# Performance work log

Measured on AMD Instinct MI355X. Metric: run time of the kernel, lower is better.

The kernel has to match this reference:

```python
import jax, jax.numpy as jnp
import numpy as np

B, N, D = 4, 2048, 512
H, HD = 8, 64  # heads, output_dim per head


def setup_inputs() -> dict:
    key = jax.random.key(0)
    ks = jax.random.split(key, 6)
    x = jax.random.normal(ks[0], (B, N, D), dtype=jnp.float32)
    adj = (jax.random.uniform(ks[1], (N, N)) < 0.1).astype(jnp.float32)
    adj = jnp.maximum(adj, jnp.eye(N, dtype=jnp.float32))
    s = 0.02
    Wq = jax.random.normal(ks[2], (D, H * HD), dtype=jnp.float32) * s
    Wk = jax.random.normal(ks[3], (D, H * HD), dtype=jnp.float32) * s
    Wv = jax.random.normal(ks[4], (D, H * HD), dtype=jnp.float32) * s
    bq = jnp.zeros((H * HD,), dtype=jnp.float32)
    bk = jnp.zeros((H * HD,), dtype=jnp.float32)
    bv = jnp.zeros((H * HD,), dtype=jnp.float32)
    return {"x": x, "adj": adj, "Wq": Wq, "bq": bq, "Wk": Wk, "bk": bk, "Wv": Wv, "bv": bv}


def reference(x, adj, Wq, bq, Wk, bk, Wv, bv):
    b, n, _ = x.shape
    q = (x @ Wq + bq).reshape(b, n, H, HD)
    k = (x @ Wk + bk).reshape(b, n, H, HD)
    v = (x @ Wv + bv).reshape(b, n, H, HD)
    # scores: [b, h, i, j]
    scores = jnp.einsum('bihd,bjhd->bhij', q, k) / jnp.sqrt(jnp.float32(HD))
    mask = jnp.where(adj == 0, jnp.float32(-1e9), jnp.float32(0.0))  # [n, n]
    scores = scores + mask[None, None, :, :]
    weights = jax.nn.softmax(scores, axis=-1)
    # dropout is identity at inference (training=False)
    out = jnp.einsum('bhij,bjhd->bihd', weights, v)
    return out.reshape(b, n, H * HD)
```

## Files before the change

kernel.cpp:

```cpp
#include <hip/hip_runtime.h>
#include <hip/hip_bf16.h>
#include <stdint.h>

#define NTOK 2048
#define DIN  512
#define QSCALE 0.18033688011112042f

typedef __attribute__((ext_vector_type(8))) short bf16x8;
typedef __attribute__((ext_vector_type(4))) short bf16x4;
typedef __attribute__((ext_vector_type(4))) float f32x4;

#define MFMA16(a, b, c) __builtin_amdgcn_mfma_f32_16x16x32_bf16((a), (b), (c), 0, 0, 0)

union u4bf8 { uint4 u; bf16x8 h; };

static __device__ __forceinline__ short f2bf(float f) {
  union { float f; uint32_t u; } v; v.f = f;
  uint32_t r = (v.u + 0x7FFFu + ((v.u >> 16) & 1u)) >> 16;
  return (short)r;
}

__global__ __launch_bounds__(256) void k_xbf(const float* __restrict__ x, short* __restrict__ xb) {
  size_t i = (size_t)blockIdx.x * 256 + threadIdx.x;
  const float4 v = *(const float4*)(x + i * 4);
  bf16x4 h;
  h[0] = f2bf(v.x); h[1] = f2bf(v.y); h[2] = f2bf(v.z); h[3] = f2bf(v.w);
  *(bf16x4*)(xb + i * 4) = h;
}

__global__ __launch_bounds__(256) void k_wt(const float* __restrict__ Wq,
                                            const float* __restrict__ Wk,
                                            const float* __restrict__ Wv,
                                            short* __restrict__ Wt) {
  const float* W = (blockIdx.z == 0) ? Wq : ((blockIdx.z == 1) ? Wk : Wv);
  short* Wo = Wt + (size_t)blockIdx.z * DIN * DIN;
  __shared__ float tile[32][33];
  int bo = blockIdx.x * 32, bc = blockIdx.y * 32;
  int tx = threadIdx.x & 31, ty = threadIdx.x >> 5;
#pragma unroll
  for (int q = 0; q < 4; ++q)
    tile[ty + q * 8][tx] = W[(bc + ty + q * 8) * DIN + bo + tx];
  __syncthreads();
#pragma unroll
  for (int q = 0; q < 4; ++q)
    Wo[(bo + ty + q * 8) * DIN + bc + tx] = f2bf(tile[tx][ty + q * 8]);
}

__global__ __launch_bounds__(256) void k_mask(const float* __restrict__ adj,
                                              unsigned long long* __restrict__ m64) {
  int wid = ((blockIdx.x * blockDim.x + threadIdx.x) >> 6);
  int lane = threadIdx.x & 63;
  int i = wid >> 5, wd = wid & 31;
  float a = adj[i * NTOK + wd * 64 + lane];
  unsigned long long b = __ballot(a != 0.0f);
  if (lane == 0) m64[i * 32 + wd] = b;
}

__global__ __launch_bounds__(256, 3) void k_qkv(const short* __restrict__ xb,
                                                const short* __restrict__ Wt,
                                                const float* __restrict__ bq,
                                                const float* __restrict__ bk,
                                                const float* __restrict__ bv,
                                                short* __restrict__ Qb, short* __restrict__ Kb,
                                                short* __restrict__ Vb) {
  __shared__ short As[2][128 * 40];
  __shared__ short Bs[2][128 * 40];
  const int z = blockIdx.z;
  const short* Wz = Wt + z * DIN * DIN;
  const float* bias = (z == 0) ? bq : ((z == 1) ? bk : bv);
  const int mbase = blockIdx.x * 128, nbase = blockIdx.y * 128;
  const int tid = threadIdx.x;
  const int lane = tid & 63, w = tid >> 6;
  const int wr = w >> 1, wc = w & 1;
  const int lrow = lane & 15, lgrp = lane >> 4;
  const int ra = tid >> 2, ca = tid & 3;

  f32x4 acc[4][4];
#pragma unroll
  for (int a = 0; a < 4; ++a)
#pragma unroll
    for (int b = 0; b < 4; ++b) acc[a][b] = (f32x4){0.f, 0.f, 0.f, 0.f};

  uint4 pA[2], pB[2];
#pragma unroll
  for (int u = 0; u < 2; ++u) {
    pA[u] = *(const uint4*)(xb + (size_t)(mbase + ra + u * 64) * DIN + ca * 8);
    pB[u] = *(const uint4*)(Wz + (size_t)(nbase + ra + u * 64) * DIN + ca * 8);
  }
#pragma unroll
  for (int u = 0; u < 2; ++u) {
    *(uint4*)(&As[0][(ra + u * 64) * 40 + ca * 8]) = pA[u];
    *(uint4*)(&Bs[0][(ra + u * 64) * 40 + ca * 8]) = pB[u];
  }
  __syncthreads();

  for (int t = 0; t < 16; ++t) {
    const int cur = t & 1, nxt = cur ^ 1;
    if (t < 15) {
      const int kb = (t + 1) * 32;
#pragma unroll
      for (int u = 0; u < 2; ++u) {
        pA[u] = *(const uint4*)(xb + (size_t)(mbase + ra + u * 64) * DIN + kb + ca * 8);
        pB[u] = *(const uint4*)(Wz + (size_t)(nbase + ra + u * 64) * DIN + kb + ca * 8);
      }
    }
    bf16x8 af[4], bf[4];
#pragma unroll
    for (int mi = 0; mi < 4; ++mi)
      af[mi] = *(bf16x8*)(&As[cur][(wr * 64 + mi * 16 + lrow) * 40 + lgrp * 8]);
#pragma unroll
    for (int ni = 0; ni < 4; ++ni)
      bf[ni] = *(bf16x8*)(&Bs[cur][(wc * 64 + ni * 16 + lrow) * 40 + lgrp * 8]);
#pragma unroll
    for (int mi = 0; mi < 4; ++mi)
#pragma unroll
      for (int ni = 0; ni < 4; ++ni) acc[mi][ni] = MFMA16(af[mi], bf[ni], acc[mi][ni]);

    if (t < 15) {
#pragma unroll
      for (int u = 0; u < 2; ++u) {
        *(uint4*)(&As[nxt][(ra + u * 64) * 40 + ca * 8]) = pA[u];
        *(uint4*)(&Bs[nxt][(ra + u * 64) * 40 + ca * 8]) = pB[u];
      }
      __syncthreads();
    }
  }

#pragma unroll
  for (int ni = 0; ni < 4; ++ni) {
    int go = nbase + wc * 64 + ni * 16 + lrow;
    float bv_ = bias[go];
    int h = go >> 6, d = go & 63;
#pragma unroll
    for (int mi = 0; mi < 4; ++mi) {
#pragma unroll
      for (int v = 0; v < 4; ++v) {
        int gm = mbase + wr * 64 + mi * 16 + lgrp * 4 + v;
        int b = gm >> 11, n = gm & 2047;
        int bh = b * 8 + h;
        float val = acc[mi][ni][v] + bv_;
        if (z == 0)
          Qb[(size_t)bh * (NTOK * 64) + n * 64 + d] = f2bf(val * QSCALE);
        else if (z == 1)
          Kb[(size_t)bh * (NTOK * 64) + n * 64 + d] = f2bf(val);
        else
          Vb[(size_t)bh * (64 * NTOK) + d * NTOK + n] = f2bf(val);
      }
    }
  }
}

__global__ __launch_bounds__(512, 8) void k_attn(const short* __restrict__ Qb,
                                                 const short* __restrict__ Kb,
                                                 const short* __restrict__ Vb,
                                                 const unsigned long long* __restrict__ m64,
                                                 float* __restrict__ out) {
  __shared__ char smem[18432];
  short* Kl = (short*)smem;
  short* Vl = (short*)(smem + 9216);
  f32x4* ored = (f32x4*)smem;
  float* lsum = (float*)(smem + 16384);

  const int itile = blockIdx.x, bh = blockIdx.y;
  const int ibase = itile * 64;
  const int tid = threadIdx.x, lane = tid & 63, w = tid >> 6;
  const int wi = w >> 1, wj = w & 1;
  const int lrow = lane & 15, lgrp = lane >> 4;

  const short* Qp = Qb + (size_t)bh * (NTOK * 64);
  const short* Kp = Kb + (size_t)bh * (NTOK * 64);
  const short* Vp = Vb + (size_t)bh * (64 * NTOK);

  const int qrow = ibase + wi * 16 + lrow;
  bf16x8 qa[2];
  qa[0] = *(const bf16x8*)(Qp + (size_t)qrow * 64 + lgrp * 8);
  qa[1] = *(const bf16x8*)(Qp + (size_t)qrow * 64 + 32 + lgrp * 8);
  const unsigned long long* mword = m64 + (size_t)qrow * 32;

  const int r0 = tid >> 3, s0 = tid & 7;

  f32x4 oacc[4];
#pragma unroll
  for (int dn = 0; dn < 4; ++dn) oacc[dn] = (f32x4){0.f, 0.f, 0.f, 0.f};
  float lrun = 0.f;

  uint4 pfK = *(const uint4*)(Kp + (size_t)r0 * 64 + s0 * 8);
  uint4 pfV = *(const uint4*)(Vp + (size_t)r0 * NTOK + s0 * 8);
  unsigned long long mw = mword[0];
  *(uint4*)(Kl + r0 * 72 + s0 * 8) = pfK;
  *(uint4*)(Vl + r0 * 72 + s0 * 8) = pfV;
  __syncthreads();

  for (int jt = 0; jt < 32; ++jt) {
    unsigned long long mwn = 0ull;
    if (jt < 31) {
      const int jn = (jt + 1) * 64;
      pfK = *(const uint4*)(Kp + (size_t)(jn + r0) * 64 + s0 * 8);
      pfV = *(const uint4*)(Vp + (size_t)r0 * NTOK + jn + s0 * 8);
      mwn = mword[jt + 1];
    }

    uint32_t pk[2][2];
#pragma unroll
    for (int jsub = 0; jsub < 2; ++jsub) {
      const int krow = (wj * 32 + jsub * 16 + lrow) * 72;
      bf16x8 kf0 = *(bf16x8*)(Kl + krow + lgrp * 8);
      bf16x8 kf1 = *(bf16x8*)(Kl + krow + 32 + lgrp * 8);
      f32x4 zz = (f32x4){0.f, 0.f, 0.f, 0.f};
      zz = MFMA16(kf0, qa[0], zz);
      zz = MFMA16(kf1, qa[1], zz);
      const uint32_t bits = (uint32_t)(mw >> (wj * 32 + jsub * 16 + lgrp * 4));
      float p0 = (bits & 1u) ? exp2f(zz[0]) : 0.f;
      float p1 = (bits & 2u) ? exp2f(zz[1]) : 0.f;
      float p2 = (bits & 4u) ? exp2f(zz[2]) : 0.f;
      float p3 = (bits & 8u) ? exp2f(zz[3]) : 0.f;
      lrun += (p0 + p1) + (p2 + p3);
      uint32_t w0, w1;
      asm("v_cvt_pk_bf16_f32 %0, %1, %2" : "=v"(w0) : "v"(p0), "v"(p1));
      asm("v_cvt_pk_bf16_f32 %0, %1, %2" : "=v"(w1) : "v"(p2), "v"(p3));
      pk[jsub][0] = w0;
      pk[jsub][1] = w1;
    }

#pragma unroll
    for (int dn = 0; dn < 4; ++dn) {
      const int vrow = (dn * 16 + lrow) * 72 + wj * 32 + lgrp * 4;
      const uint2 v0 = *(const uint2*)(Vl + vrow);
      const uint2 v1 = *(const uint2*)(Vl + vrow + 16);
      u4bf8 vb;
      vb.u = (uint4){v0.x, v0.y, v1.x, v1.y};
      u4bf8 pa;
      pa.u = (uint4){pk[0][0], pk[0][1], pk[1][0], pk[1][1]};
      oacc[dn] = MFMA16(pa.h, vb.h, oacc[dn]);
    }

    if (jt < 31) {
      __syncthreads();
      *(uint4*)(Kl + r0 * 72 + s0 * 8) = pfK;
      *(uint4*)(Vl + r0 * 72 + s0 * 8) = pfV;
      mw = mwn;
      __syncthreads();
    }
  }

  __syncthreads();

  {
    float s = lrun;
    s += __shfl_xor(s, 16);
    s += __shfl_xor(s, 32);
    if (lane < 16) lsum[w * 16 + lane] = s;
  }
  if (wj == 1) {
#pragma unroll
    for (int dn = 0; dn < 4; ++dn) ored[(wi * 4 + dn) * 64 + lane] = oacc[dn];
  }
  __syncthreads();

  if (wj == 0) {
    const int b = bh >> 3, h = bh & 7;
    const f32x4 la = *(const f32x4*)&lsum[(wi * 2 + 0) * 16 + lgrp * 4];
    const f32x4 lb = *(const f32x4*)&lsum[(wi * 2 + 1) * 16 + lgrp * 4];
    float inv[4];
#pragma unroll
    for (int v = 0; v < 4; ++v) inv[v] = 1.0f / (la[v] + lb[v]);
#pragma unroll
    for (int dn = 0; dn < 4; ++dn) {
      f32x4 s = oacc[dn] + ored[(wi * 4 + dn) * 64 + lane];
#pragma unroll
      for (int v = 0; v < 4; ++v) {
        int i = ibase + wi * 16 + lgrp * 4 + v;
        out[(size_t)(b * NTOK + i) * DIN + h * 64 + dn * 16 + lrow] = s[v] * inv[v];
      }
    }
  }
}

extern "C" void kernel_launch(void* const* d_in, const int* in_sizes, int n_in,
                              void* d_out, int out_size, void* d_ws, size_t ws_size,
                              hipStream_t stream) {
  const float* x   = (const float*)d_in[0];
  const float* adj = (const float*)d_in[1];
  const float* Wq  = (const float*)d_in[2];
  const float* bq  = (const float*)d_in[3];
  const float* Wk  = (const float*)d_in[4];
  const float* bk  = (const float*)d_in[5];
  const float* Wv  = (const float*)d_in[6];
  const float* bv  = (const float*)d_in[7];
  float* out = (float*)d_out;

  char* ws = (char*)d_ws;
  short* Qb = (short*)(ws);
  short* Kb = (short*)(ws + (8u << 20));
  short* Vb = (short*)(ws + (16u << 20));
  short* Wt = (short*)(ws + (24u << 20));
  unsigned long long* m64 = (unsigned long long*)(ws + (26u << 20));
  short* xb = (short*)d_out;

  k_xbf<<<4096, 256, 0, stream>>>(x, xb);
  k_wt<<<dim3(16, 16, 3), 256, 0, stream>>>(Wq, Wk, Wv, Wt);
  k_mask<<<16384, 256, 0, stream>>>(adj, m64);
  k_qkv<<<dim3(64, 4, 3), 256, 0, stream>>>(xb, Wt, bq, bk, bv, Qb, Kb, Vb);
  k_attn<<<dim3(32, 32), 512, 0, stream>>>(Qb, Kb, Vb, m64, out);
}
```

Before: 115.3 us.

## Double key tile per barrier, XOR-swizzle LDS, remap block order for locality

The attention kernel now stages 128 keys and values per iteration in two halves, which halves the barrier count and issues more global prefetch per step. It replaces the padded 72-stride LDS layout with a dense 64-stride layout that uses an XOR swizzle to avoid bank conflicts. Blocks are launched on a 1D grid whose index is remapped so that neighbouring blocks fall on different batch-heads, aiming to spread L2 and channel traffic. In exchange LDS grows to 32KB per block, which may lower occupancy, and registers rise from the extra prefetch.

```diff
diff --git a/kernel.cpp b/kernel.cpp
--- a/kernel.cpp
+++ b/kernel.cpp
@@ -155,13 +155,15 @@
                                                  const short* __restrict__ Vb,
                                                  const unsigned long long* __restrict__ m64,
                                                  float* __restrict__ out) {
-  __shared__ char smem[18432];
-  short* Kl = (short*)smem;
-  short* Vl = (short*)(smem + 9216);
+  __shared__ char smem[32768];
+  short* Ks = (short*)smem;
+  short* Vs = (short*)smem + 8192;
   f32x4* ored = (f32x4*)smem;
   float* lsum = (float*)(smem + 16384);
 
-  const int itile = blockIdx.x, bh = blockIdx.y;
+  const int bid = blockIdx.x;
+  const int bh = (bid & 7) * 4 + ((bid >> 3) & 3);
+  const int itile = bid >> 5;
   const int ibase = itile * 64;
   const int tid = threadIdx.x, lane = tid & 63, w = tid >> 6;
   const int wi = w >> 1, wj = w & 1;
@@ -178,67 +180,90 @@
   const unsigned long long* mword = m64 + (size_t)qrow * 32;
 
   const int r0 = tid >> 3, s0 = tid & 7;
+  const int ksw = (s0 ^ (r0 & 7)) * 8;
 
   f32x4 oacc[4];
 #pragma unroll
   for (int dn = 0; dn < 4; ++dn) oacc[dn] = (f32x4){0.f, 0.f, 0.f, 0.f};
   float lrun = 0.f;
 
-  uint4 pfK = *(const uint4*)(Kp + (size_t)r0 * 64 + s0 * 8);
-  uint4 pfV = *(const uint4*)(Vp + (size_t)r0 * NTOK + s0 * 8);
-  unsigned long long mw = mword[0];
-  *(uint4*)(Kl + r0 * 72 + s0 * 8) = pfK;
-  *(uint4*)(Vl + r0 * 72 + s0 * 8) = pfV;
-  __syncthreads();
-
-  for (int jt = 0; jt < 32; ++jt) {
-    unsigned long long mwn = 0ull;
-    if (jt < 31) {
-      const int jn = (jt + 1) * 64;
-      pfK = *(const uint4*)(Kp + (size_t)(jn + r0) * 64 + s0 * 8);
-      pfV = *(const uint4*)(Vp + (size_t)r0 * NTOK + jn + s0 * 8);
-      mwn = mword[jt + 1];
-    }
-
-    uint32_t pk[2][2];
-#pragma unroll
-    for (int jsub = 0; jsub < 2; ++jsub) {
-      const int krow = (wj * 32 + jsub * 16 + lrow) * 72;
-      bf16x8 kf0 = *(bf16x8*)(Kl + krow + lgrp * 8);
-      bf16x8 kf1 = *(bf16x8*)(Kl + krow + 32 + lgrp * 8);
-      f32x4 zz = (f32x4){0.f, 0.f, 0.f, 0.f};
-      zz = MFMA16(kf0, qa[0], zz);
-      zz = MFMA16(kf1, qa[1], zz);
-      const uint32_t bits = (uint32_t)(mw >> (wj * 32 + jsub * 16 + lgrp * 4));
-      float p0 = (bits & 1u) ? exp2f(zz[0]) : 0.f;
-      float p1 = (bits & 2u) ? exp2f(zz[1]) : 0.f;
-      float p2 = (bits & 4u) ? exp2f(zz[2]) : 0.f;
-      float p3 = (bits & 8u) ? exp2f(zz[3]) : 0.f;
-      lrun += (p0 + p1) + (p2 + p3);
-      uint32_t w0, w1;
-      asm("v_cvt_pk_bf16_f32 %0, %1, %2" : "=v"(w0) : "v"(p0), "v"(p1));
-      asm("v_cvt_pk_bf16_f32 %0, %1, %2" : "=v"(w1) : "v"(p2), "v"(p3));
-      pk[jsub][0] = w0;
-      pk[jsub][1] = w1;
-    }
-
-#pragma unroll
-    for (int dn = 0; dn < 4; ++dn) {
-      const int vrow = (dn * 16 + lrow) * 72 + wj * 32 + lgrp * 4;
-      const uint2 v0 = *(const uint2*)(Vl + vrow);
-      const uint2 v1 = *(const uint2*)(Vl + vrow + 16);
-      u4bf8 vb;
-      vb.u = (uint4){v0.x, v0.y, v1.x, v1.y};
-      u4bf8 pa;
-      pa.u = (uint4){pk[0][0], pk[0][1], pk[1][0], pk[1][1]};
-      oacc[dn] = MFMA16(pa.h, vb.h, oacc[dn]);
-    }
-
-    if (jt < 31) {
+  const int r3 = lrow & 7;
+
+  uint4 pfK0 = *(const uint4*)(Kp + (size_t)r0 * 64 + s0 * 8);
+  uint4 pfK1 = *(const uint4*)(Kp + (size_t)(r0 + 64) * 64 + s0 * 8);
+  uint4 pfV0 = *(const uint4*)(Vp + (size_t)r0 * NTOK + s0 * 8);
+  uint4 pfV1 = *(const uint4*)(Vp + (size_t)r0 * NTOK + 64 + s0 * 8);
+  unsigned long long mw0 = mword[0], mw1 = mword[1];
+  *(uint4*)(Ks + r0 * 64 + ksw) = pfK0;
+  *(uint4*)(Ks + (r0 + 64) * 64 + ksw) = pfK1;
+  *(uint4*)(Vs + r0 * 64 + ksw) = pfV0;
+  *(uint4*)(Vs + 4096 + r0 * 64 + ksw) = pfV1;
+  __syncthreads();
+
+  for (int jp = 0; jp < 16; ++jp) {
+    unsigned long long mwn0 = 0ull, mwn1 = 0ull;
+    if (jp < 15) {
+      const int jb = (jp + 1) * 128;
+      pfK0 = *(const uint4*)(Kp + (size_t)(jb + r0) * 64 + s0 * 8);
+      pfK1 = *(const uint4*)(Kp + (size_t)(jb + r0 + 64) * 64 + s0 * 8);
+      pfV0 = *(const uint4*)(Vp + (size_t)r0 * NTOK + jb + s0 * 8);
+      pfV1 = *(const uint4*)(Vp + (size_t)r0 * NTOK + jb + 64 + s0 * 8);
+      mwn0 = mword[jp * 2 + 2];
+      mwn1 = mword[jp * 2 + 3];
+    }
+
+#pragma unroll
+    for (int half = 0; half < 2; ++half) {
+      const short* Kh = Ks + half * 4096;
+      const short* Vh = Vs + half * 4096;
+      const unsigned long long mw = half ? mw1 : mw0;
+
+      uint32_t pk[2][2];
+#pragma unroll
+      for (int jsub = 0; jsub < 2; ++jsub) {
+        const int R = wj * 32 + jsub * 16 + lrow;
+        bf16x8 kf0 = *(bf16x8*)(Kh + R * 64 + ((lgrp ^ r3) * 8));
+        bf16x8 kf1 = *(bf16x8*)(Kh + R * 64 + (((4 + lgrp) ^ r3) * 8));
+        f32x4 zz = (f32x4){0.f, 0.f, 0.f, 0.f};
+        zz = MFMA16(kf0, qa[0], zz);
+        zz = MFMA16(kf1, qa[1], zz);
+        const uint32_t bits = (uint32_t)(mw >> (wj * 32 + jsub * 16 + lgrp * 4));
+        float p0 = (bits & 1u) ? exp2f(zz[0]) : 0.f;
+        float p1 = (bits & 2u) ? exp2f(zz[1]) : 0.f;
+        float p2 = (bits & 4u) ? exp2f(zz[2]) : 0.f;
+        float p3 = (bits & 8u) ? exp2f(zz[3]) : 0.f;
+        lrun += (p0 + p1) + (p2 + p3);
+        uint32_t w0, w1;
+        asm("v_cvt_pk_bf16_f32 %0, %1, %2" : "=v"(w0) : "v"(p0), "v"(p1));
+        asm("v_cvt_pk_bf16_f32 %0, %1, %2" : "=v"(w1) : "v"(p2), "v"(p3));
+        pk[jsub][0] = w0;
+        pk[jsub][1] = w1;
+      }
+
+      const int g1 = lgrp >> 1, g0 = (lgrp & 1) * 4;
+      const int c8a = (wj * 4 + g1) ^ r3;
+      const int c8b = (wj * 4 + 2 + g1) ^ r3;
+#pragma unroll
+      for (int dn = 0; dn < 4; ++dn) {
+        const int vrow = (dn * 16 + lrow) * 64;
+        const uint2 v0 = *(const uint2*)(Vh + vrow + c8a * 8 + g0);
+        const uint2 v1 = *(const uint2*)(Vh + vrow + c8b * 8 + g0);
+        u4bf8 vb;
+        vb.u = (uint4){v0.x, v0.y, v1.x, v1.y};
+        u4bf8 pa;
+        pa.u = (uint4){pk[0][0], pk[0][1], pk[1][0], pk[1][1]};
+        oacc[dn] = MFMA16(pa.h, vb.h, oacc[dn]);
+      }
+    }
+
+    if (jp < 15) {
       __syncthreads();
-      *(uint4*)(Kl + r0 * 72 + s0 * 8) = pfK;
-      *(uint4*)(Vl + r0 * 72 + s0 * 8) = pfV;
-      mw = mwn;
+      *(uint4*)(Ks + r0 * 64 + ksw) = pfK0;
+      *(uint4*)(Ks + (r0 + 64) * 64 + ksw) = pfK1;
+      *(uint4*)(Vs + r0 * 64 + ksw) = pfV0;
+      *(uint4*)(Vs + 4096 + r0 * 64 + ksw) = pfV1;
+      mw0 = mwn0;
+      mw1 = mwn1;
       __syncthreads();
     }
   }
@@ -301,5 +326,5 @@
   k_wt<<<dim3(16, 16, 3), 256, 0, stream>>>(Wq, Wk, Wv, Wt);
   k_mask<<<16384, 256, 0, stream>>>(adj, m64);
   k_qkv<<<dim3(64, 4, 3), 256, 0, stream>>>(xb, Wt, bq, bk, bv, Qb, Kb, Vb);
-  k_attn<<<dim3(32, 32), 512, 0, stream>>>(Qb, Kb, Vb, m64, out);
-}
+  k_attn<<<1024, 512, 0, stream>>>(Qb, Kb, Vb, m64, out);
+}
```

After: 291.8 us. 2.53x slower.
